# Kernel tuning notes

Measured on AMD Instinct MI355X. Metric: run time of the kernel, lower is better.

The kernel has to match this reference:

```python
import jax, jax.numpy as jnp
import numpy as np

N_STEPS = 128
N_UNITS = 2048
BATCH = 256
DT = 1e-3
TAU_M = 10.0 * DT            # NeuroTorch LIFLayer default tau_m
ALPHA = float(np.exp(-DT / TAU_M))  # membrane decay factor
THRESHOLD = 1.0
GAMMA = 100.0                # surrogate-gradient sharpness


@jax.custom_vjp
def heaviside_spike(v):
    # forward: hard threshold; backward: sigmoid surrogate (see fwdbwd module)
    return (v > THRESHOLD).astype(v.dtype)

def _hs_fwd(v):
    return heaviside_spike(v), v

def _hs_bwd(v, g):
    sig = jax.nn.sigmoid(GAMMA * (v - THRESHOLD))
    return (g * GAMMA * sig * (1.0 - sig),)

heaviside_spike.defvjp(_hs_fwd, _hs_bwd)


def setup_inputs() -> dict:
    key = jax.random.key(0)
    kx, kw = jax.random.split(key)
    x = jax.random.normal(kx, (BATCH, N_UNITS), dtype=jnp.float32)
    # LIF feedforward weights (n_units -> n_units), no recurrent connection
    W = (jax.random.normal(kw, (N_UNITS, N_UNITS), dtype=jnp.float32)
         / np.float32(np.sqrt(N_UNITS)))
    return {"x": x, "W": W}


def reference(x, W):
    # x: (B, N) analog input; first "spike" frame is the raw input (as in source).
    def step(carry, _):
        x_fwd, V, Z = carry
        I = x_fwd @ W                                   # (B, N)
        # reset term uses detached spikes in the original (stop_gradient)
        V_next = ALPHA * V * (1.0 - jax.lax.stop_gradient(Z)) + I
        Z_next = heaviside_spike(V_next)
        return (Z_next, V_next, Z_next), Z_next

    V0 = jnp.zeros_like(x)
    Z0 = jnp.zeros_like(x)
    _, spikes = jax.lax.scan(step, (x, V0, Z0), None, length=N_STEPS - 1)
    # spikes: (n_steps-1, B, N); prepend the analog frame -> stack along time
    out = jnp.concatenate([x[None], spikes], axis=0)    # (T, B, N)
    return jnp.transpose(out, (1, 0, 2))                # (B, T, N)
```

## Files before the change

### kernel.cpp

```cpp
#include <hip/hip_runtime.h>
#include <stdint.h>


#define BATCHSZ 256
#define NU      2048
#define TSTEPS  128
#define BLK     1024
#define NWAVES  (BLK / 64)

#define A_BM 8
#define A_BN 128

__global__ __launch_bounds__(256) void lif_dense_v1(
    const float* __restrict__ x,
    const float* __restrict__ W,
    float* __restrict__ ws)
{
    __shared__ float s_x[A_BM][NU];

    const int tid = threadIdx.x;
    const int n0  = blockIdx.x * A_BN;
    const int m0  = blockIdx.y * A_BM;

    {
        const int r = tid >> 5;
        const int l = tid & 31;
        const float* xr = x + (size_t)(m0 + r) * NU;
        #pragma unroll
        for (int j = 0; j < 16; ++j) {
            int col = l * 4 + j * 128;
            float4 v = *(const float4*)(xr + col);
            *(float4*)&s_x[r][col] = v;
        }
    }
    __syncthreads();

    const int mg    = tid >> 5;
    const int nlane = tid & 31;
    const int n     = n0 + nlane * 4;

    const float* xr = &s_x[mg][0];
    const float* wp = W + n;

    float4 acc; acc.x = acc.y = acc.z = acc.w = 0.0f;

    #pragma unroll 8
    for (int k = 0; k < NU; ++k) {
        float  xk = xr[k];
        float4 wv = *(const float4*)(wp + (size_t)k * NU);
        acc.x = __builtin_fmaf(xk, wv.x, acc.x);
        acc.y = __builtin_fmaf(xk, wv.y, acc.y);
        acc.z = __builtin_fmaf(xk, wv.z, acc.z);
        acc.w = __builtin_fmaf(xk, wv.w, acc.w);
    }

    *(float4*)&ws[(size_t)(m0 + mg) * NU + n] = acc;
}

__global__ __launch_bounds__(BLK) void lif_recurrence(
    const float* __restrict__ x,
    const float* __restrict__ W,
    const float* __restrict__ V1,
    float* __restrict__ out)
{
    const int b    = blockIdx.x;
    const int tid  = threadIdx.x;
    const int lane = tid & 63;
    const int wid  = tid >> 6;

    __shared__ int           s_idx[NU];
    __shared__ unsigned char s_flag[NU];
    __shared__ int           s_wsum[NWAVES];
    __shared__ int           s_cnt;

    const int n0 = tid;
    const int n1 = tid + BLK;

    float* outb = out + (size_t)b * TSTEPS * NU;

    float V0, V1r;
    int   z0, z1;
    {
        float x0 = x[(size_t)b * NU + n0];
        float x1 = x[(size_t)b * NU + n1];
        outb[n0] = x0;
        outb[n1] = x1;
        V0  = V1[(size_t)b * NU + n0];
        V1r = V1[(size_t)b * NU + n1];
        z0 = V0  > 1.0f;
        z1 = V1r > 1.0f;
        float* f1 = outb + NU;
        f1[n0] = z0 ? 1.0f : 0.0f;
        f1[n1] = z1 ? 1.0f : 0.0f;
        s_flag[n0] = (unsigned char)z0;
        s_flag[n1] = (unsigned char)z1;
    }
    __syncthreads();

    for (int t = 2; t < TSTEPS; ++t) {
        int f0 = s_flag[2 * tid];
        int f1 = s_flag[2 * tid + 1];
        int c  = f0 + f1;
        int v  = c;
        #pragma unroll
        for (int d = 1; d < 64; d <<= 1) {
            int o = __shfl_up(v, d);
            if (lane >= d) v += o;
        }
        if (lane == 63) s_wsum[wid] = v;
        __syncthreads();
        int base = 0;
        #pragma unroll
        for (int w = 0; w < NWAVES; ++w) base += (w < wid) ? s_wsum[w] : 0;
        int off = base + v - c;
        if (f0) s_idx[off++] = (2 * tid) * NU;
        if (f1) s_idx[off]   = (2 * tid + 1) * NU;
        if (tid == BLK - 1) s_cnt = base + v;
        __syncthreads();

        int cnt = s_cnt;
        if (cnt == 0) {
            size_t  elems  = (size_t)(TSTEPS - t) * NU;
            float4* p      = (float4*)(outb + (size_t)t * NU);
            int     chunks = (int)(elems / 4);
            float4  zz; zz.x = zz.y = zz.z = zz.w = 0.0f;
            for (int i = tid; i < chunks; i += BLK) p[i] = zz;
            return;
        }

        float I0 = 0.0f, I1 = 0.0f;
        const float* Wc = W + tid;
        int i = 0;
        for (; i + 4 <= cnt; i += 4) {
            const float* r0 = Wc + s_idx[i];
            const float* r1 = Wc + s_idx[i + 1];
            const float* r2 = Wc + s_idx[i + 2];
            const float* r3 = Wc + s_idx[i + 3];
            float a0 = r0[0], b0 = r0[BLK];
            float a1 = r1[0], b1 = r1[BLK];
            float a2 = r2[0], b2 = r2[BLK];
            float a3 = r3[0], b3 = r3[BLK];
            I0 += a0; I0 += a1; I0 += a2; I0 += a3;
            I1 += b0; I1 += b1; I1 += b2; I1 += b3;
        }
        for (; i < cnt; ++i) {
            const float* r = Wc + s_idx[i];
            I0 += r[0];
            I1 += r[BLK];
        }

        float d0 = 0.90483741803595952f * V0;
        float d1 = 0.90483741803595952f * V1r;
        asm volatile("" : "+v"(d0), "+v"(d1));
        float nv0 = (z0 ? 0.0f : d0) + I0;
        float nv1 = (z1 ? 0.0f : d1) + I1;
        V0 = nv0; V1r = nv1;
        z0 = nv0 > 1.0f;
        z1 = nv1 > 1.0f;

        float* po = outb + (size_t)t * NU;
        po[n0] = z0 ? 1.0f : 0.0f;
        po[n1] = z1 ? 1.0f : 0.0f;
        s_flag[n0] = (unsigned char)z0;
        s_flag[n1] = (unsigned char)z1;
        __syncthreads();
    }
}

__global__ __launch_bounds__(BLK) void lif_fused(
    const float* __restrict__ x,
    const float* __restrict__ W,
    float* __restrict__ out)
{
    const int b    = blockIdx.x;
    const int tid  = threadIdx.x;
    const int lane = tid & 63;
    const int wid  = tid >> 6;

    __shared__ float         s_x[NU];
    __shared__ int           s_idx[NU];
    __shared__ unsigned char s_flag[NU];
    __shared__ int           s_wsum[NWAVES];
    __shared__ int           s_cnt;

    const int n0 = tid;
    const int n1 = tid + BLK;
    float* outb = out + (size_t)b * TSTEPS * NU;

    {
        float x0 = x[(size_t)b * NU + n0];
        float x1 = x[(size_t)b * NU + n1];
        s_x[n0] = x0; s_x[n1] = x1;
        outb[n0] = x0; outb[n1] = x1;
    }
    __syncthreads();

    float I0 = 0.0f, I1 = 0.0f;
    {
        const float* Wc = W + tid;
        #pragma unroll 8
        for (int k = 0; k < NU; ++k) {
            float xk = s_x[k];
            const float* wr = Wc + (size_t)k * NU;
            I0 = __builtin_fmaf(xk, wr[0],   I0);
            I1 = __builtin_fmaf(xk, wr[BLK], I1);
        }
    }

    float V0 = 0.0f, V1 = 0.0f;
    int   z0 = 0,    z1 = 0;

    for (int t = 1; t < TSTEPS; ++t) {
        if (t >= 2) {
            int f0 = s_flag[2 * tid];
            int f1 = s_flag[2 * tid + 1];
            int c  = f0 + f1;
            int v  = c;
            #pragma unroll
            for (int d = 1; d < 64; d <<= 1) {
                int o = __shfl_up(v, d);
                if (lane >= d) v += o;
            }
            if (lane == 63) s_wsum[wid] = v;
            __syncthreads();
            int base = 0;
            #pragma unroll
            for (int w = 0; w < NWAVES; ++w) base += (w < wid) ? s_wsum[w] : 0;
            int off = base + v - c;
            if (f0) s_idx[off++] = 2 * tid;
            if (f1) s_idx[off]   = 2 * tid + 1;
            if (tid == BLK - 1) s_cnt = base + v;
            __syncthreads();

            int cnt = s_cnt;
            if (cnt == 0) {
                size_t  elems  = (size_t)(TSTEPS - t) * NU;
                float4* p      = (float4*)(outb + (size_t)t * NU);
                int     chunks = (int)(elems / 4);
                float4  zz; zz.x = zz.y = zz.z = zz.w = 0.0f;
                for (int i = tid; i < chunks; i += BLK) p[i] = zz;
                return;
            }

            I0 = 0.0f; I1 = 0.0f;
            const float* Wc = W + tid;
            int i = 0;
            for (; i + 2 <= cnt; i += 2) {
                const float* r0 = Wc + (size_t)s_idx[i]     * NU;
                const float* r1 = Wc + (size_t)s_idx[i + 1] * NU;
                float a0 = r0[0], b0 = r0[BLK];
                float a1 = r1[0], b1 = r1[BLK];
                I0 += a0; I0 += a1;
                I1 += b0; I1 += b1;
            }
            for (; i < cnt; ++i) {
                const float* r = Wc + (size_t)s_idx[i] * NU;
                I0 += r[0];
                I1 += r[BLK];
            }
        }

        float d0 = 0.90483741803595952f * V0;
        float d1 = 0.90483741803595952f * V1;
        asm volatile("" : "+v"(d0), "+v"(d1));
        float nv0 = (z0 ? 0.0f : d0) + I0;
        float nv1 = (z1 ? 0.0f : d1) + I1;
        V0 = nv0; V1 = nv1;
        z0 = nv0 > 1.0f;
        z1 = nv1 > 1.0f;

        float* po = outb + (size_t)t * NU;
        po[n0] = z0 ? 1.0f : 0.0f;
        po[n1] = z1 ? 1.0f : 0.0f;
        s_flag[n0] = (unsigned char)z0;
        s_flag[n1] = (unsigned char)z1;
        __syncthreads();
    }
}

extern "C" void kernel_launch(void* const* d_in, const int* in_sizes, int n_in,
                              void* d_out, int out_size, void* d_ws, size_t ws_size,
                              hipStream_t stream) {
    const float* x = (const float*)d_in[0];
    const float* W = (const float*)d_in[1];
    if (n_in >= 2 && in_sizes[0] == NU * NU && in_sizes[1] == BATCHSZ * NU) {
        const float* t = x; x = W; W = t;
    }
    float* out = (float*)d_out;

    const size_t need = (size_t)BATCHSZ * NU * sizeof(float);
    if (ws_size >= need) {
        float* V1 = (float*)d_ws;
        hipLaunchKernelGGL(lif_dense_v1,
                           dim3(NU / A_BN, BATCHSZ / A_BM), dim3(256), 0, stream,
                           x, W, V1);
        hipLaunchKernelGGL(lif_recurrence,
                           dim3(BATCHSZ), dim3(BLK), 0, stream,
                           x, W, V1, out);
    } else {
        hipLaunchKernelGGL(lif_fused, dim3(BATCHSZ), dim3(BLK), 0, stream,
                           x, W, out);
    }
}
```

Measured before the change: 209.6 us.

## Restructure first-step dense GEMM kernel: 512 threads, float2 columns, batched W loads

Rewrites the first-step x@W kernel to use 512 threads per block, each computing two output columns instead of four, and swaps the grid order so consecutive blocks share the same W column slab. The k loop is restructured to read 16 x values as float4 from shared memory and issue 16 independent W loads before the FMAs, aiming for more memory-level parallelism and better L2 reuse of W. Narrower float2 loads give less bytes per instruction and may reduce coalescing efficiency.

Measured after the change: 316.9 us. 1.51x slower.

```diff
diff --git a/kernel.cpp b/kernel.cpp
--- a/kernel.cpp
+++ b/kernel.cpp
@@ -10,8 +10,9 @@
 
 #define A_BM 8
 #define A_BN 128
-
-__global__ __launch_bounds__(256) void lif_dense_v1(
+#define A_THR 512
+
+__global__ __launch_bounds__(A_THR) void lif_dense_v1(
     const float* __restrict__ x,
     const float* __restrict__ W,
     float* __restrict__ ws)
@@ -19,42 +20,55 @@
     __shared__ float s_x[A_BM][NU];
 
     const int tid = threadIdx.x;
-    const int n0  = blockIdx.x * A_BN;
-    const int m0  = blockIdx.y * A_BM;
+    const int m0  = blockIdx.x * A_BM;
+    const int n0  = blockIdx.y * A_BN;
 
     {
-        const int r = tid >> 5;
-        const int l = tid & 31;
-        const float* xr = x + (size_t)(m0 + r) * NU;
-        #pragma unroll
-        for (int j = 0; j < 16; ++j) {
-            int col = l * 4 + j * 128;
-            float4 v = *(const float4*)(xr + col);
-            *(float4*)&s_x[r][col] = v;
+        const int w = tid >> 6;
+        const int l = tid & 63;
+        const float* xr = x + (size_t)(m0 + w) * NU;
+        float*       dr = &s_x[w][0];
+        #pragma unroll
+        for (int it = 0; it < 8; ++it) {
+            int col = it * 256 + l * 4;
+            *(float4*)&dr[col] = *(const float4*)&xr[col];
         }
     }
     __syncthreads();
 
-    const int mg    = tid >> 5;
-    const int nlane = tid & 31;
-    const int n     = n0 + nlane * 4;
+    const int mg = tid >> 6;
+    const int cg = tid & 63;
+    const int n  = n0 + cg * 2;
 
     const float* xr = &s_x[mg][0];
     const float* wp = W + n;
 
-    float4 acc; acc.x = acc.y = acc.z = acc.w = 0.0f;
-
-    #pragma unroll 8
-    for (int k = 0; k < NU; ++k) {
-        float  xk = xr[k];
-        float4 wv = *(const float4*)(wp + (size_t)k * NU);
-        acc.x = __builtin_fmaf(xk, wv.x, acc.x);
-        acc.y = __builtin_fmaf(xk, wv.y, acc.y);
-        acc.z = __builtin_fmaf(xk, wv.z, acc.z);
-        acc.w = __builtin_fmaf(xk, wv.w, acc.w);
-    }
-
-    *(float4*)&ws[(size_t)(m0 + mg) * NU + n] = acc;
+    float2 acc; acc.x = 0.0f; acc.y = 0.0f;
+
+    for (int k0 = 0; k0 < NU; k0 += 16) {
+        float4 x0 = *(const float4*)&xr[k0 + 0];
+        float4 x1 = *(const float4*)&xr[k0 + 4];
+        float4 x2 = *(const float4*)&xr[k0 + 8];
+        float4 x3 = *(const float4*)&xr[k0 + 12];
+        float xs[16];
+        xs[ 0] = x0.x; xs[ 1] = x0.y; xs[ 2] = x0.z; xs[ 3] = x0.w;
+        xs[ 4] = x1.x; xs[ 5] = x1.y; xs[ 6] = x1.z; xs[ 7] = x1.w;
+        xs[ 8] = x2.x; xs[ 9] = x2.y; xs[10] = x2.z; xs[11] = x2.w;
+        xs[12] = x3.x; xs[13] = x3.y; xs[14] = x3.z; xs[15] = x3.w;
+
+        float2 wv[16];
+        #pragma unroll
+        for (int j = 0; j < 16; ++j)
+            wv[j] = *(const float2*)(wp + (size_t)(k0 + j) * NU);
+
+        #pragma unroll
+        for (int j = 0; j < 16; ++j) {
+            acc.x = __builtin_fmaf(xs[j], wv[j].x, acc.x);
+            acc.y = __builtin_fmaf(xs[j], wv[j].y, acc.y);
+        }
+    }
+
+    *(float2*)&ws[(size_t)(m0 + mg) * NU + n] = acc;
 }
 
 __global__ __launch_bounds__(BLK) void lif_recurrence(
@@ -292,7 +306,7 @@
     if (ws_size >= need) {
         float* V1 = (float*)d_ws;
         hipLaunchKernelGGL(lif_dense_v1,
-                           dim3(NU / A_BN, BATCHSZ / A_BM), dim3(256), 0, stream,
+                           dim3(BATCHSZ / A_BM, NU / A_BN), dim3(A_THR), 0, stream,
                            x, W, V1);
         hipLaunchKernelGGL(lif_recurrence,
                            dim3(BATCHSZ), dim3(BLK), 0, stream,
```

## Retile dense first-step GEMM with double-buffered shared W tiles and register blocking

Applied to the files above, without the earlier changes.

Rewrites the initial x@W kernel so each block stages 32x64 tiles of W through double-buffered shared memory with register prefetch. Each thread now computes 8 output rows for one column, reading x as wave-uniform float4 loads. Before, every thread streamed W straight from global memory once per batch row. The goal is more reuse of W per load and overlap of the next tile's global load with compute, in exchange for smaller blocks and a per-tile barrier.

Measured after the change: 359.6 us. 71.5% more time.

```diff
diff --git a/kernel.cpp b/kernel.cpp
--- a/kernel.cpp
+++ b/kernel.cpp
@@ -8,53 +8,82 @@
 #define BLK     1024
 #define NWAVES  (BLK / 64)
 
-#define A_BM 8
-#define A_BN 128
-
-__global__ __launch_bounds__(256) void lif_dense_v1(
+#define A_BK 32
+#define A_NT (NU / A_BK)
+
+__global__ __launch_bounds__(128) void lif_dense_v1(
     const float* __restrict__ x,
     const float* __restrict__ W,
     float* __restrict__ ws)
 {
-    __shared__ float s_x[A_BM][NU];
-
-    const int tid = threadIdx.x;
-    const int n0  = blockIdx.x * A_BN;
-    const int m0  = blockIdx.y * A_BM;
-
-    {
-        const int r = tid >> 5;
-        const int l = tid & 31;
-        const float* xr = x + (size_t)(m0 + r) * NU;
-        #pragma unroll
-        for (int j = 0; j < 16; ++j) {
-            int col = l * 4 + j * 128;
-            float4 v = *(const float4*)(xr + col);
-            *(float4*)&s_x[r][col] = v;
-        }
-    }
+    __shared__ float s_w[2][A_BK * 64];
+
+    const int tid  = threadIdx.x;
+    const int lane = tid & 63;
+    const int n0   = blockIdx.x * 64;
+    const int m0   = blockIdx.y * 16;
+
+    const int wu = __builtin_amdgcn_readfirstlane(tid >> 6);
+    const float* xp = x + (size_t)(m0 + 8 * wu) * NU;
+
+    float4 pf[4];
+
+    auto stage_load = [&](int t) {
+        const float* src = W + (size_t)(t * A_BK) * NU + n0;
+        #pragma unroll
+        for (int j = 0; j < 4; ++j) {
+            int f   = j * 128 + tid;
+            int row = f >> 4;
+            int c4  = f & 15;
+            pf[j] = *(const float4*)(src + (size_t)row * NU + c4 * 4);
+        }
+    };
+    auto stage_write = [&](int buf) {
+        float4* dst = (float4*)&s_w[buf][0];
+        #pragma unroll
+        for (int j = 0; j < 4; ++j) dst[j * 128 + tid] = pf[j];
+    };
+
+    stage_load(0);
+    stage_write(0);
     __syncthreads();
-
-    const int mg    = tid >> 5;
-    const int nlane = tid & 31;
-    const int n     = n0 + nlane * 4;
-
-    const float* xr = &s_x[mg][0];
-    const float* wp = W + n;
-
-    float4 acc; acc.x = acc.y = acc.z = acc.w = 0.0f;
-
-    #pragma unroll 8
-    for (int k = 0; k < NU; ++k) {
-        float  xk = xr[k];
-        float4 wv = *(const float4*)(wp + (size_t)k * NU);
-        acc.x = __builtin_fmaf(xk, wv.x, acc.x);
-        acc.y = __builtin_fmaf(xk, wv.y, acc.y);
-        acc.z = __builtin_fmaf(xk, wv.z, acc.z);
-        acc.w = __builtin_fmaf(xk, wv.w, acc.w);
-    }
-
-    *(float4*)&ws[(size_t)(m0 + mg) * NU + n] = acc;
+    stage_load(1);
+
+    float acc[8];
+    #pragma unroll
+    for (int r = 0; r < 8; ++r) acc[r] = 0.0f;
+
+    for (int t = 0; t < A_NT; ++t) {
+        const float* wt = &s_w[t & 1][0];
+        const int    kb = t * A_BK;
+
+        #pragma unroll
+        for (int k4 = 0; k4 < A_BK / 4; ++k4) {
+            float4 xq[8];
+            #pragma unroll
+            for (int r = 0; r < 8; ++r)
+                xq[r] = *(const float4*)(xp + (size_t)r * NU + kb + k4 * 4);
+            const float* xqf = (const float*)&xq[0];
+
+            #pragma unroll
+            for (int kk = 0; kk < 4; ++kk) {
+                float wv = wt[(k4 * 4 + kk) * 64 + lane];
+                #pragma unroll
+                for (int r = 0; r < 8; ++r)
+                    acc[r] = __builtin_fmaf(xqf[r * 4 + kk], wv, acc[r]);
+            }
+        }
+
+        if (t + 1 < A_NT) {
+            stage_write((t + 1) & 1);
+            __syncthreads();
+            if (t + 2 < A_NT) stage_load(t + 2);
+        }
+    }
+
+    #pragma unroll
+    for (int r = 0; r < 8; ++r)
+        ws[(size_t)(m0 + 8 * wu + r) * NU + n0 + lane] = acc[r];
 }
 
 __global__ __launch_bounds__(BLK) void lif_recurrence(
@@ -292,7 +321,7 @@
     if (ws_size >= need) {
         float* V1 = (float*)d_ws;
         hipLaunchKernelGGL(lif_dense_v1,
-                           dim3(NU / A_BN, BATCHSZ / A_BM), dim3(256), 0, stream,
+                           dim3(NU / 64, BATCHSZ / 16), dim3(128), 0, stream,
                            x, W, V1);
         hipLaunchKernelGGL(lif_recurrence,
                            dim3(BATCHSZ), dim3(BLK), 0, stream,
```

## Restructure first-step dense GEMM with register tiling and double-buffered W loads

Applied to the files above, without the earlier changes.

Rewrites the initial x@W kernel so each wave computes two batch rows and reads x straight from global memory through a wave-uniform scalar pointer instead of staging it in shared memory. W rows are prefetched into two register buffers of eight float4s, so loads for the next chunk overlap the FMAs on the current one. The tile and grid shapes change to 4 rows by 256 columns per 128-thread block. This removes the shared-memory staging and the barrier, and each W load now feeds two rows. In exchange it uses more registers and gives fewer threads per block.

After: 185.4 us. 1.13x faster.

```diff
diff --git a/kernel.cpp b/kernel.cpp
--- a/kernel.cpp
+++ b/kernel.cpp
@@ -8,53 +8,77 @@
 #define BLK     1024
 #define NWAVES  (BLK / 64)
 
-#define A_BM 8
-#define A_BN 128
-
-__global__ __launch_bounds__(256) void lif_dense_v1(
+
+__global__ __launch_bounds__(128) void lif_dense_v1(
     const float* __restrict__ x,
     const float* __restrict__ W,
     float* __restrict__ ws)
 {
-    __shared__ float s_x[A_BM][NU];
-
-    const int tid = threadIdx.x;
-    const int n0  = blockIdx.x * A_BN;
-    const int m0  = blockIdx.y * A_BM;
-
-    {
-        const int r = tid >> 5;
-        const int l = tid & 31;
-        const float* xr = x + (size_t)(m0 + r) * NU;
-        #pragma unroll
-        for (int j = 0; j < 16; ++j) {
-            int col = l * 4 + j * 128;
-            float4 v = *(const float4*)(xr + col);
-            *(float4*)&s_x[r][col] = v;
-        }
-    }
-    __syncthreads();
-
-    const int mg    = tid >> 5;
-    const int nlane = tid & 31;
-    const int n     = n0 + nlane * 4;
-
-    const float* xr = &s_x[mg][0];
-    const float* wp = W + n;
-
-    float4 acc; acc.x = acc.y = acc.z = acc.w = 0.0f;
-
-    #pragma unroll 8
-    for (int k = 0; k < NU; ++k) {
-        float  xk = xr[k];
-        float4 wv = *(const float4*)(wp + (size_t)k * NU);
-        acc.x = __builtin_fmaf(xk, wv.x, acc.x);
-        acc.y = __builtin_fmaf(xk, wv.y, acc.y);
-        acc.z = __builtin_fmaf(xk, wv.z, acc.z);
-        acc.w = __builtin_fmaf(xk, wv.w, acc.w);
-    }
-
-    *(float4*)&ws[(size_t)(m0 + mg) * NU + n] = acc;
+    const int tid  = threadIdx.x;
+    const int lane = tid & 63;
+    const int n0   = blockIdx.x * 256;
+    const int m0   = blockIdx.y * 4;
+
+    const int rb = __builtin_amdgcn_readfirstlane((tid >> 6) * 2);
+    const float* x0p = x + (size_t)(m0 + rb) * NU;
+    const float* x1p = x0p + NU;
+
+    const float* wp = W + n0 + lane * 4;
+
+    float4 bA[8], bB[8];
+    float acc0[4] = {0.f, 0.f, 0.f, 0.f};
+    float acc1[4] = {0.f, 0.f, 0.f, 0.f};
+
+    #pragma unroll
+    for (int j = 0; j < 8; ++j)
+        bA[j] = *(const float4*)(wp + (size_t)j * NU);
+
+    for (int k0 = 0; k0 < NU; k0 += 16) {
+        #pragma unroll
+        for (int j = 0; j < 8; ++j)
+            bB[j] = *(const float4*)(wp + (size_t)(k0 + 8 + j) * NU);
+
+        #pragma unroll
+        for (int j = 0; j < 8; ++j) {
+            float  xa = x0p[k0 + j];
+            float  xb = x1p[k0 + j];
+            float4 wv = bA[j];
+            acc0[0] = __builtin_fmaf(xa, wv.x, acc0[0]);
+            acc0[1] = __builtin_fmaf(xa, wv.y, acc0[1]);
+            acc0[2] = __builtin_fmaf(xa, wv.z, acc0[2]);
+            acc0[3] = __builtin_fmaf(xa, wv.w, acc0[3]);
+            acc1[0] = __builtin_fmaf(xb, wv.x, acc1[0]);
+            acc1[1] = __builtin_fmaf(xb, wv.y, acc1[1]);
+            acc1[2] = __builtin_fmaf(xb, wv.z, acc1[2]);
+            acc1[3] = __builtin_fmaf(xb, wv.w, acc1[3]);
+        }
+
+        if (k0 + 16 < NU) {
+            #pragma unroll
+            for (int j = 0; j < 8; ++j)
+                bA[j] = *(const float4*)(wp + (size_t)(k0 + 16 + j) * NU);
+        }
+
+        #pragma unroll
+        for (int j = 0; j < 8; ++j) {
+            float  xa = x0p[k0 + 8 + j];
+            float  xb = x1p[k0 + 8 + j];
+            float4 wv = bB[j];
+            acc0[0] = __builtin_fmaf(xa, wv.x, acc0[0]);
+            acc0[1] = __builtin_fmaf(xa, wv.y, acc0[1]);
+            acc0[2] = __builtin_fmaf(xa, wv.z, acc0[2]);
+            acc0[3] = __builtin_fmaf(xa, wv.w, acc0[3]);
+            acc1[0] = __builtin_fmaf(xb, wv.x, acc1[0]);
+            acc1[1] = __builtin_fmaf(xb, wv.y, acc1[1]);
+            acc1[2] = __builtin_fmaf(xb, wv.z, acc1[2]);
+            acc1[3] = __builtin_fmaf(xb, wv.w, acc1[3]);
+        }
+    }
+
+    float4 o0; o0.x = acc0[0]; o0.y = acc0[1]; o0.z = acc0[2]; o0.w = acc0[3];
+    float4 o1; o1.x = acc1[0]; o1.y = acc1[1]; o1.z = acc1[2]; o1.w = acc1[3];
+    *(float4*)&ws[(size_t)(m0 + rb)     * NU + n0 + lane * 4] = o0;
+    *(float4*)&ws[(size_t)(m0 + rb + 1) * NU + n0 + lane * 4] = o1;
 }
 
 __global__ __launch_bounds__(BLK) void lif_recurrence(
@@ -292,7 +316,7 @@
     if (ws_size >= need) {
         float* V1 = (float*)d_ws;
         hipLaunchKernelGGL(lif_dense_v1,
-                           dim3(NU / A_BN, BATCHSZ / A_BM), dim3(256), 0, stream,
+                           dim3(NU / 256, BATCHSZ / 4), dim3(128), 0, stream,
                            x, W, V1);
         hipLaunchKernelGGL(lif_recurrence,
                            dim3(BATCHSZ), dim3(BLK), 0, stream,
```
